# Kernel optimization log

Hardware: AMD Instinct MI355X
Metric: run time of the kernel (lower is better)

Reference implementation:

```python
import jax, jax.numpy as jnp
import numpy as np

B, N, L, D, DP, H = 1, 128, 256, 256, 128, 8
DH = D // H
LN_EPS = 1e-5


def setup_inputs() -> dict:
    key = jax.random.key(0)
    ks = jax.random.split(key, 8)
    w = lambda k, shape: jax.random.normal(k, shape, jnp.float32) * 0.02
    return {
        "msa": jax.random.normal(ks[0], (B, N, L, D), jnp.float32),
        "pair_bias": jax.random.normal(ks[1], (B, L, L, DP), jnp.float32),
        "msa_mask": jnp.ones((B, N, L), jnp.int32),
        "ln_g": jnp.ones((D,), jnp.float32),
        "ln_b": jnp.zeros((D,), jnp.float32),
        "Wq": w(ks[2], (D, D)), "bq": jnp.zeros((D,), jnp.float32),
        "Wk": w(ks[3], (D, D)), "bk": jnp.zeros((D,), jnp.float32),
        "Wv": w(ks[4], (D, D)), "bv": jnp.zeros((D,), jnp.float32),
        "Wb": w(ks[5], (DP, H)), "bb": jnp.zeros((H,), jnp.float32),
        "Wo": w(ks[6], (D, D)), "bo": jnp.zeros((D,), jnp.float32),
        # gate initialized as in the torch module: zero weight, ones bias
        "Wg": jnp.zeros((D, D), jnp.float32), "bg": jnp.ones((D,), jnp.float32),
    }


def reference(msa, pair_bias, msa_mask, ln_g, ln_b, Wq, bq, Wk, bk, Wv, bv,
              Wb, bb, Wo, bo, Wg, bg):
    b, n, l, d = msa.shape
    h = bb.shape[0]
    dh = d // h
    # LayerNorm over d_msa
    mu = msa.mean(-1, keepdims=True)
    var = msa.var(-1, keepdims=True)
    xn = (msa - mu) * jax.lax.rsqrt(var + LN_EPS) * ln_g + ln_b
    # projections -> [b, n, l, h, dh]
    q = (xn @ Wq + bq).reshape(b, n, l, h, dh)
    k = (xn @ Wk + bk).reshape(b, n, l, h, dh)
    v = (xn @ Wv + bv).reshape(b, n, l, h, dh)
    scores = jnp.einsum('bnihd,bnjhd->bnhij', q, k) / jnp.sqrt(jnp.float32(dh))
    # pair bias: [b, l, l, h] -> [b, 1, h, l, l], broadcast over N_seq
    bias = (pair_bias @ Wb + bb).transpose(0, 3, 1, 2)[:, None]
    scores = scores + bias
    # mask over key axis
    mask = msa_mask[:, :, None, None, :].astype(bool)
    scores = jnp.where(mask, scores, jnp.float32(-1e9))
    attn = jax.nn.softmax(scores, axis=-1)  # dropout is identity at eval
    out = jnp.einsum('bnhij,bnjhd->bnihd', attn, v).reshape(b, n, l, d)
    out = out @ Wo + bo
    gate = jax.nn.sigmoid(xn @ Wg + bg)
    return out * gate
```

## Files before the change

kernel.cpp:

```cpp
#include <hip/hip_runtime.h>
#include <hip/hip_bf16.h>

typedef __attribute__((ext_vector_type(4))) float f32x4;
typedef __attribute__((ext_vector_type(16))) float f32x16;
typedef __attribute__((ext_vector_type(8))) __bf16 bf16x8;
typedef __attribute__((ext_vector_type(4))) __bf16 bf16x4;
typedef __attribute__((ext_vector_type(2))) __bf16 bf16x2;
typedef __attribute__((ext_vector_type(4))) unsigned u32x4;
typedef __attribute__((ext_vector_type(2))) unsigned u32x2;

#define VTS 264
#define KLS 40
#define L2E 1.4426950408889634f

#define GLOAD_LDS16(g, l) __builtin_amdgcn_global_load_lds( \
    (const __attribute__((address_space(1))) void*)(g),     \
    (__attribute__((address_space(3))) void*)(l), 16, 0, 0)

#if __has_builtin(__builtin_amdgcn_permlane32_swap)
#define SWP(a, b) { u32x2 _r = __builtin_amdgcn_permlane32_swap((a), (b), false, false); \
                    (a) = _r[0]; (b) = _r[1]; }
#else
#define SWP(a, b) { unsigned _sa = __shfl_xor((a), 32), _sb = __shfl_xor((b), 32); \
                    unsigned _na = hi ? _sb : (a); (b) = hi ? (b) : _sa; (a) = _na; }
#endif
#define SUM32(ts, lrun) { (lrun) += (ts) + __shfl_xor((ts), 32); }

__global__ __launch_bounds__(256) void setup_kernel(
    const float* __restrict__ msa, const float* __restrict__ g,
    const float* __restrict__ b, __bf16* __restrict__ xn,
    const float* __restrict__ pair, const float* __restrict__ Wb,
    const float* __restrict__ bb, float* __restrict__ biasP,
    const float* __restrict__ Wq, const float* __restrict__ Wk,
    const float* __restrict__ Wv, const float* __restrict__ Wg,
    const float* __restrict__ Wo, __bf16* __restrict__ Wt)
{
  __shared__ float wbs[1024];
  const int bid = blockIdx.x;
  const int t = threadIdx.x;
  if (bid < 8192) {
    const int row = bid * 4 + (t >> 6);
    const int lane = t & 63;
    f32x4 x = *(const f32x4*)(msa + (size_t)row * 256 + lane * 4);
    float s = x[0] + x[1] + x[2] + x[3];
    float s2 = x[0]*x[0] + x[1]*x[1] + x[2]*x[2] + x[3]*x[3];
#pragma unroll
    for (int d = 32; d >= 1; d >>= 1) {
      s  += __shfl_xor(s, d);
      s2 += __shfl_xor(s2, d);
    }
    const float mu  = s * (1.f / 256.f);
    const float inv = rsqrtf(s2 * (1.f / 256.f) - mu * mu + 1e-5f);
    const f32x4 gv = *(const f32x4*)(g + lane * 4);
    const f32x4 bv = *(const f32x4*)(b + lane * 4);
    bf16x4 o;
#pragma unroll
    for (int j = 0; j < 4; ++j) o[j] = (__bf16)((x[j] - mu) * inv * gv[j] + bv[j]);
    *(bf16x4*)(xn + (size_t)row * 256 + lane * 4) = o;
  } else if (bid < 8448) {
#pragma unroll
    for (int r2 = 0; r2 < 4; ++r2) wbs[t + 256 * r2] = Wb[t + 256 * r2];
    __syncthreads();
    const int i = bid - 8192, j = t;
    const float* src = pair + ((size_t)i * 256 + j) * 128;
    float acc[8];
#pragma unroll
    for (int hh = 0; hh < 8; ++hh) acc[hh] = bb[hh];
    for (int p = 0; p < 128; p += 4) {
      const f32x4 pv = *(const f32x4*)(src + p);
#pragma unroll
      for (int q2 = 0; q2 < 4; ++q2)
#pragma unroll
        for (int hh = 0; hh < 8; ++hh) acc[hh] += pv[q2] * wbs[(p + q2) * 8 + hh];
    }
    const int kt2 = j >> 5, g2 = (j >> 3) & 3, h2 = (j >> 2) & 1, e2 = j & 3;
#pragma unroll
    for (int hh = 0; hh < 8; ++hh)
      biasP[(((((size_t)hh * 8 + kt2) * 4 + g2) * 2 + h2) * 256 + i) * 4 + e2] =
          acc[hh] * L2E;
  } else {
    const int idx = bid - 8448;
    const int w = idx >> 8, n2 = idx & 255, k = t;
    const float* W = (w == 0) ? Wq : (w == 1) ? Wk : (w == 2) ? Wv : (w == 3) ? Wg : Wo;
    Wt[((size_t)w * 256 + n2) * 256 + k] = (__bf16)W[(size_t)k * 256 + n2];
  }
}

__global__ __launch_bounds__(512, 4) void qkvg_gemm(
    const __bf16* __restrict__ xn, const __bf16* __restrict__ Wt,
    const float* __restrict__ bq, const float* __restrict__ bk,
    const float* __restrict__ bv, const float* __restrict__ bg,
    __bf16* __restrict__ qb, __bf16* __restrict__ kb,
    __bf16* __restrict__ vb, __bf16* __restrict__ gateb)
{
  __shared__ alignas(16) __bf16 Al[256 * 64];
  __shared__ alignas(16) __bf16 Bl[128 * 64];
  const int t = threadIdx.x;
  const int wave = t >> 6, lane = t & 63;
  const int l15 = lane & 15, l16 = lane >> 4;
  const int bid = blockIdx.x;
  const int xcd = bid & 7, idx = bid >> 3;
  const int m0 = (xcd * 16 + (idx & 15)) * 256;
  const int bn = idx >> 4;
  const int w = bn >> 1;
  const int nloc0 = (bn & 1) * 128;
  const __bf16* Wtw = Wt + (size_t)w * 65536;
  const int wm = (wave >> 1) * 64, wn = (wave & 1) * 64;

  const int srow = (lane >> 3);
  const int chunk = ((lane & 7) ^ srow) * 8;

  f32x4 acc[4][4];
#pragma unroll
  for (int i = 0; i < 4; ++i)
#pragma unroll
    for (int j = 0; j < 4; ++j) acc[i][j] = (f32x4){0.f, 0.f, 0.f, 0.f};

  for (int kt = 0; kt < 4; ++kt) {
    const int k0 = kt * 64;
#pragma unroll
    for (int i = 0; i < 4; ++i) {
      const int row = (wave * 4 + i) * 8 + srow;
      GLOAD_LDS16(xn + (size_t)(m0 + row) * 256 + k0 + chunk, &Al[(wave * 4 + i) * 512]);
    }
#pragma unroll
    for (int i = 0; i < 2; ++i) {
      const int row = (wave * 2 + i) * 8 + srow;
      GLOAD_LDS16(Wtw + (size_t)(nloc0 + row) * 256 + k0 + chunk, &Bl[(wave * 2 + i) * 512]);
    }
    __syncthreads();
#pragma unroll
    for (int kk = 0; kk < 2; ++kk) {
      bf16x8 a[4], bfr[4];
#pragma unroll
      for (int mi = 0; mi < 4; ++mi) {
        const int row = wm + mi * 16 + l15;
        a[mi] = *(const bf16x8*)&Al[row * 64 + ((kk * 32 + l16 * 8) ^ ((row & 7) << 3))];
      }
#pragma unroll
      for (int ni = 0; ni < 4; ++ni) {
        const int row = wn + ni * 16 + l15;
        bfr[ni] = *(const bf16x8*)&Bl[row * 64 + ((kk * 32 + l16 * 8) ^ ((row & 7) << 3))];
      }
#pragma unroll
      for (int mi = 0; mi < 4; ++mi)
#pragma unroll
        for (int ni = 0; ni < 4; ++ni)
          acc[mi][ni] = __builtin_amdgcn_mfma_f32_16x16x32_bf16(a[mi], bfr[ni], acc[mi][ni], 0, 0, 0);
    }
    __syncthreads();
  }

  const float* bias_arr = (w == 0) ? bq : (w == 1) ? bk : (w == 2) ? bv : bg;
  float bnis[4];
#pragma unroll
  for (int ni = 0; ni < 4; ++ni) bnis[ni] = bias_arr[nloc0 + wn + ni * 16 + l15];
  const float qscale = 0.17677669529663687f * L2E;

#pragma unroll
  for (int mi = 0; mi < 4; ++mi)
#pragma unroll
    for (int ni = 0; ni < 4; ++ni)
#pragma unroll
      for (int r = 0; r < 4; ++r) {
        const int grow = m0 + wm + mi * 16 + l16 * 4 + r;
        const int gcol = nloc0 + wn + ni * 16 + l15;
        const float v = acc[mi][ni][r] + bnis[ni];
        const int n = grow >> 8, i2 = grow & 255, h = gcol >> 5, dh = gcol & 31;
        const size_t hoff = (((size_t)n * 8 + h) * 256 + i2) * 32 + dh;
        if (w == 0)      qb[hoff] = (__bf16)(v * qscale);
        else if (w == 1) kb[hoff] = (__bf16)v;
        else if (w == 2) vb[hoff] = (__bf16)v;
        else gateb[(size_t)grow * 256 + gcol] = (__bf16)(1.f / (1.f + __expf(-v)));
      }
}

__device__ __forceinline__ unsigned pk2(float a, float b) {
  bf16x2 t; t[0] = (__bf16)a; t[1] = (__bf16)b;
  return __builtin_bit_cast(unsigned, t);
}

__global__ __launch_bounds__(512, 4) void attn_kernel(
    const __bf16* __restrict__ qb, const __bf16* __restrict__ kb,
    const __bf16* __restrict__ vb, const float* __restrict__ biasP,
    const int* __restrict__ mask, __bf16* __restrict__ opre)
{
  __shared__ alignas(16) __bf16 Kl[256 * KLS];
  __shared__ alignas(16) __bf16 Vt[32 * VTS];
  __shared__ alignas(16) float Ml[256];
  const int t = threadIdx.x, wave = t >> 6, lane = t & 63;
  const int l31 = lane & 31, hi = lane >> 5;
  const int nh = blockIdx.x;
  const int n = nh >> 3, h = nh & 7;
  const __bf16* qbh = qb + (size_t)nh * 8192;

  if (t < 256) {
    const bf16x8* ks = (const bf16x8*)(kb + (size_t)nh * 8192 + t * 32);
    bf16x8 kr[4];
#pragma unroll
    for (int j = 0; j < 4; ++j) kr[j] = ks[j];
#pragma unroll
    for (int j = 0; j < 4; ++j) *(bf16x8*)&Kl[t * KLS + j * 8] = kr[j];
    const bf16x8* vs = (const bf16x8*)(vb + (size_t)nh * 8192 + t * 32);
    bf16x8 vv[4];
#pragma unroll
    for (int j = 0; j < 4; ++j) vv[j] = vs[j];
#pragma unroll
    for (int j = 0; j < 4; ++j)
#pragma unroll
      for (int e = 0; e < 8; ++e) Vt[(j * 8 + e) * VTS + t] = vv[j][e];
    Ml[t] = mask[n * 256 + t] ? 0.f : -1e9f;
  }
  __syncthreads();

  const int q0 = wave * 32;
  const int q = q0 + l31;
  const bf16x8 Qf0 = *(const bf16x8*)(qbh + (size_t)q * 32 + hi * 8);
  const bf16x8 Qf1 = *(const bf16x8*)(qbh + (size_t)q * 32 + 16 + hi * 8);

  const float* bph = biasP + (size_t)h * 65536;

  f32x4 bc[4];
#pragma unroll
  for (int g = 0; g < 4; ++g) {
    const f32x4 bv = *(const f32x4*)(bph + ((g * 2 + hi) * 256 + q) * 4);
    const f32x4 mk = *(const f32x4*)&Ml[8 * g + 4 * hi];
    bc[g] = bv + mk;
  }

  f32x16 Ot;
#pragma unroll
  for (int r = 0; r < 16; ++r) Ot[r] = 0.f;
  float lrun = 0.f;

#pragma unroll 1
  for (int kt = 0; kt < 8; ++kt) {
    const int k0 = kt * 32;
    const int ktn = (kt + 1) & 7;
    const bf16x8 Kf0 = *(const bf16x8*)&Kl[(k0 + l31) * KLS + hi * 8];
    const bf16x8 Kf1 = *(const bf16x8*)&Kl[(k0 + l31) * KLS + 16 + hi * 8];
    const bf16x8 Vf0 = *(const bf16x8*)&Vt[l31 * VTS + k0 + hi * 8];
    const bf16x8 Vf1 = *(const bf16x8*)&Vt[l31 * VTS + k0 + 16 + hi * 8];
    f32x16 st;
#pragma unroll
    for (int g = 0; g < 4; ++g)
#pragma unroll
      for (int e = 0; e < 4; ++e) st[4 * g + e] = bc[g][e];
    st = __builtin_amdgcn_mfma_f32_32x32x16_bf16(Kf0, Qf0, st, 0, 0, 0);
    st = __builtin_amdgcn_mfma_f32_32x32x16_bf16(Kf1, Qf1, st, 0, 0, 0);
#pragma unroll
    for (int g = 0; g < 4; ++g) {
      const f32x4 bv = *(const f32x4*)(bph + (((ktn * 4 + g) * 2 + hi) * 256 + q) * 4);
      const f32x4 mk = *(const f32x4*)&Ml[ktn * 32 + 8 * g + 4 * hi];
      bc[g] = bv + mk;
    }
#pragma unroll
    for (int r = 0; r < 16; ++r) st[r] = exp2f(st[r]);
    float ts = st[0];
#pragma unroll
    for (int r = 1; r < 16; ++r) ts += st[r];
    SUM32(ts, lrun);
    unsigned c0 = pk2(st[0],  st[1]),  c1 = pk2(st[2],  st[3]);
    unsigned c2 = pk2(st[4],  st[5]),  c3 = pk2(st[6],  st[7]);
    unsigned c4 = pk2(st[8],  st[9]),  c5 = pk2(st[10], st[11]);
    unsigned c6 = pk2(st[12], st[13]), c7 = pk2(st[14], st[15]);
    SWP(c0, c2); SWP(c1, c3); SWP(c4, c6); SWP(c5, c7);
    u32x4 w0 = {c0, c1, c2, c3}, w1 = {c4, c5, c6, c7};
    const bf16x8 pf0 = __builtin_bit_cast(bf16x8, w0);
    const bf16x8 pf1 = __builtin_bit_cast(bf16x8, w1);
    Ot = __builtin_amdgcn_mfma_f32_32x32x16_bf16(Vf0, pf0, Ot, 0, 0, 0);
    Ot = __builtin_amdgcn_mfma_f32_32x32x16_bf16(Vf1, pf1, Ot, 0, 0, 0);
  }

  const float invl = 1.f / lrun;
  unsigned P00 = pk2(Ot[0]  * invl, Ot[1]  * invl), P01 = pk2(Ot[2]  * invl, Ot[3]  * invl);
  unsigned P10 = pk2(Ot[4]  * invl, Ot[5]  * invl), P11 = pk2(Ot[6]  * invl, Ot[7]  * invl);
  unsigned P20 = pk2(Ot[8]  * invl, Ot[9]  * invl), P21 = pk2(Ot[10] * invl, Ot[11] * invl);
  unsigned P30 = pk2(Ot[12] * invl, Ot[13] * invl), P31 = pk2(Ot[14] * invl, Ot[15] * invl);
  SWP(P00, P20); SWP(P01, P21); SWP(P10, P30); SWP(P11, P31);
  u32x4 s0 = {P00, P01, P20, P21}, s1 = {P10, P11, P30, P31};
  __bf16* dst = opre + (((size_t)h * 128 + n) * 256 + q) * 32 + hi * 16;
  *(u32x4*)dst = s0;
  *(u32x4*)(dst + 8) = s1;
}

__global__ __launch_bounds__(256) void wo_gemm(
    const __bf16* __restrict__ A, const __bf16* __restrict__ Wtw,
    const float* __restrict__ bo, const __bf16* __restrict__ gateb,
    float* __restrict__ out)
{
  __shared__ alignas(16) __bf16 Al[128 * 64];
  __shared__ alignas(16) __bf16 Bl[128 * 64];
  const int t = threadIdx.x;
  const int wave = t >> 6, lane = t & 63;
  const int l15 = lane & 15, l16 = lane >> 4;
  const int bid = blockIdx.x;
  const int xcd = bid & 7, idx = bid >> 3;
  const int m0 = (xcd * 32 + (idx & 31)) * 128;
  const int nloc0 = (idx >> 5) * 128;
  const int wm = (wave >> 1) * 64, wn = (wave & 1) * 64;

  const int srow = (lane >> 3);
  const int chunk = ((lane & 7) ^ srow) * 8;

  f32x4 acc[4][4];
#pragma unroll
  for (int i = 0; i < 4; ++i)
#pragma unroll
    for (int j = 0; j < 4; ++j) acc[i][j] = (f32x4){0.f, 0.f, 0.f, 0.f};

  for (int kt = 0; kt < 4; ++kt) {
    const int k0 = kt * 64;
#pragma unroll
    for (int i = 0; i < 4; ++i) {
      const int row = wave * 32 + i * 8 + srow;
      const int m = m0 + row;
      const int kg = k0 + chunk;
      GLOAD_LDS16(A + (size_t)(kg >> 5) * 1048576 + (size_t)(m >> 8) * 8192
                    + (m & 255) * 32 + (kg & 31),
                  &Al[(wave * 4 + i) * 512]);
      GLOAD_LDS16(Wtw + (size_t)(nloc0 + row) * 256 + kg, &Bl[(wave * 4 + i) * 512]);
    }
    __syncthreads();
#pragma unroll
    for (int kk = 0; kk < 2; ++kk) {
      bf16x8 a[4], bfr[4];
#pragma unroll
      for (int mi = 0; mi < 4; ++mi) {
        const int row = wm + mi * 16 + l15;
        a[mi] = *(const bf16x8*)&Al[row * 64 + ((kk * 32 + l16 * 8) ^ ((row & 7) << 3))];
      }
#pragma unroll
      for (int ni = 0; ni < 4; ++ni) {
        const int row = wn + ni * 16 + l15;
        bfr[ni] = *(const bf16x8*)&Bl[row * 64 + ((kk * 32 + l16 * 8) ^ ((row & 7) << 3))];
      }
#pragma unroll
      for (int mi = 0; mi < 4; ++mi)
#pragma unroll
        for (int ni = 0; ni < 4; ++ni)
          acc[mi][ni] = __builtin_amdgcn_mfma_f32_16x16x32_bf16(a[mi], bfr[ni], acc[mi][ni], 0, 0, 0);
    }
    __syncthreads();
  }

  float bov[4];
#pragma unroll
  for (int ni = 0; ni < 4; ++ni) bov[ni] = bo[nloc0 + wn + ni * 16 + l15];
#pragma unroll
  for (int mi = 0; mi < 4; ++mi)
#pragma unroll
    for (int ni = 0; ni < 4; ++ni)
#pragma unroll
      for (int r = 0; r < 4; ++r) {
        const int grow = m0 + wm + mi * 16 + l16 * 4 + r;
        const int gcol = nloc0 + wn + ni * 16 + l15;
        const size_t o = (size_t)grow * 256 + gcol;
        out[o] = (acc[mi][ni][r] + bov[ni]) * (float)gateb[o];
      }
}

extern "C" void kernel_launch(void* const* d_in, const int* in_sizes, int n_in,
                              void* d_out, int out_size, void* d_ws, size_t ws_size,
                              hipStream_t stream)
{
  const float* msa  = (const float*)d_in[0];
  const float* pair = (const float*)d_in[1];
  const int*   mask = (const int*)d_in[2];
  const float* ln_g = (const float*)d_in[3];
  const float* ln_b = (const float*)d_in[4];
  const float* Wq = (const float*)d_in[5];  const float* bq = (const float*)d_in[6];
  const float* Wk = (const float*)d_in[7];  const float* bk = (const float*)d_in[8];
  const float* Wv = (const float*)d_in[9];  const float* bv = (const float*)d_in[10];
  const float* Wb = (const float*)d_in[11]; const float* bb = (const float*)d_in[12];
  const float* Wo = (const float*)d_in[13]; const float* bo = (const float*)d_in[14];
  const float* Wg = (const float*)d_in[15]; const float* bg = (const float*)d_in[16];
  float* out = (float*)d_out;

  char* ws = (char*)d_ws;
  __bf16* xn    = (__bf16*)(ws);
  __bf16* qb    = (__bf16*)(ws + 16777216);
  __bf16* kb    = (__bf16*)(ws + 2 * 16777216);
  __bf16* vb    = (__bf16*)(ws + 3 * 16777216);
  __bf16* opre  = (__bf16*)(ws + 4 * 16777216);
  __bf16* Wt    = (__bf16*)(ws + 5 * 16777216);
  __bf16* gateb = (__bf16*)(ws + 5 * 16777216 + 655360);
  float*  biasP = (float*)(ws + 5 * 16777216 + 655360 + 16777216);

  hipLaunchKernelGGL(setup_kernel, dim3(9728), dim3(256), 0, stream,
                     msa, ln_g, ln_b, xn, pair, Wb, bb, biasP, Wq, Wk, Wv, Wg, Wo, Wt);
  hipLaunchKernelGGL(qkvg_gemm,   dim3(1024), dim3(512), 0, stream, xn, Wt, bq, bk, bv, bg, qb, kb, vb, gateb);
  hipLaunchKernelGGL(attn_kernel, dim3(1024), dim3(512), 0, stream, qb, kb, vb, biasP, mask, opre);
  hipLaunchKernelGGL(wo_gemm,     dim3(512),  dim3(256), 0, stream, opre, Wt + 4 * 65536, bo, gateb, out);
}
```

Before: 114.3 us.

## Split pair-bias projection across 8 lanes per row with shuffle reduction

After: 112.3 us. Within noise of the previous version (-1.7%).

```diff
diff --git a/kernel.cpp b/kernel.cpp
--- a/kernel.cpp
+++ b/kernel.cpp
@@ -57,29 +57,42 @@
 #pragma unroll
     for (int j = 0; j < 4; ++j) o[j] = (__bf16)((x[j] - mu) * inv * gv[j] + bv[j]);
     *(bf16x4*)(xn + (size_t)row * 256 + lane * 4) = o;
-  } else if (bid < 8448) {
+  } else if (bid < 10240) {
 #pragma unroll
     for (int r2 = 0; r2 < 4; ++r2) wbs[t + 256 * r2] = Wb[t + 256 * r2];
     __syncthreads();
-    const int i = bid - 8192, j = t;
-    const float* src = pair + ((size_t)i * 256 + j) * 128;
+    const int rb = (bid - 8192) * 32 + (t >> 3);
+    const int g8 = t & 7;
+    const float* src = pair + (size_t)rb * 128 + g8 * 16;
+    f32x4 pv[4];
+#pragma unroll
+    for (int c = 0; c < 4; ++c) pv[c] = *(const f32x4*)(src + c * 4);
     float acc[8];
 #pragma unroll
-    for (int hh = 0; hh < 8; ++hh) acc[hh] = bb[hh];
-    for (int p = 0; p < 128; p += 4) {
-      const f32x4 pv = *(const f32x4*)(src + p);
-#pragma unroll
-      for (int q2 = 0; q2 < 4; ++q2)
-#pragma unroll
-        for (int hh = 0; hh < 8; ++hh) acc[hh] += pv[q2] * wbs[(p + q2) * 8 + hh];
-    }
+    for (int hh = 0; hh < 8; ++hh) acc[hh] = 0.f;
+#pragma unroll
+    for (int c = 0; c < 4; ++c)
+#pragma unroll
+      for (int e = 0; e < 4; ++e) {
+        const int p = g8 * 16 + c * 4 + e;
+        const f32x4 w0 = *(const f32x4*)&wbs[p * 8];
+        const f32x4 w1 = *(const f32x4*)&wbs[p * 8 + 4];
+#pragma unroll
+        for (int hh = 0; hh < 4; ++hh) {
+          acc[hh]     += pv[c][e] * w0[hh];
+          acc[4 + hh] += pv[c][e] * w1[hh];
+        }
+      }
+#pragma unroll
+    for (int d = 1; d <= 4; d <<= 1)
+#pragma unroll
+      for (int hh = 0; hh < 8; ++hh) acc[hh] += __shfl_xor(acc[hh], d);
+    const int i = rb >> 8, j = rb & 255;
     const int kt2 = j >> 5, g2 = (j >> 3) & 3, h2 = (j >> 2) & 1, e2 = j & 3;
-#pragma unroll
-    for (int hh = 0; hh < 8; ++hh)
-      biasP[(((((size_t)hh * 8 + kt2) * 4 + g2) * 2 + h2) * 256 + i) * 4 + e2] =
-          acc[hh] * L2E;
+    biasP[(((((size_t)g8 * 8 + kt2) * 4 + g2) * 2 + h2) * 256 + i) * 4 + e2] =
+        (acc[g8] + bb[g8]) * L2E;
   } else {
-    const int idx = bid - 8448;
+    const int idx = bid - 10240;
     const int w = idx >> 8, n2 = idx & 255, k = t;
     const float* W = (w == 0) ? Wq : (w == 1) ? Wk : (w == 2) ? Wv : (w == 3) ? Wg : Wo;
     Wt[((size_t)w * 256 + n2) * 256 + k] = (__bf16)W[(size_t)k * 256 + n2];
@@ -387,7 +400,7 @@
   __bf16* gateb = (__bf16*)(ws + 5 * 16777216 + 655360);
   float*  biasP = (float*)(ws + 5 * 16777216 + 655360 + 16777216);
 
-  hipLaunchKernelGGL(setup_kernel, dim3(9728), dim3(256), 0, stream,
+  hipLaunchKernelGGL(setup_kernel, dim3(11520), dim3(256), 0, stream,
                      msa, ln_g, ln_b, xn, pair, Wb, bb, biasP, Wq, Wk, Wv, Wg, Wo, Wt);
   hipLaunchKernelGGL(qkvg_gemm,   dim3(1024), dim3(512), 0, stream, xn, Wt, bq, bk, bv, bg, qb, kb, vb, gateb);
   hipLaunchKernelGGL(attn_kernel, dim3(1024), dim3(512), 0, stream, qb, kb, vb, biasP, mask, opre);
```
